# Performance work log

Measured on AMD Instinct MI355X. Metric: run time of the kernel, lower is better.

Reference implementation:

```python
import jax, jax.numpy as jnp
import numpy as np

D_MODEL = 1024
NUM_HEADS = 16
D_K = D_MODEL // NUM_HEADS


def setup_inputs() -> dict:
    key = jax.random.key(0)
    ks = jax.random.split(key, 11)
    s = 1.0 / np.sqrt(D_MODEL)
    inp = {
        "Q": jax.random.normal(ks[0], (2, 2048, D_MODEL), jnp.float32),
        "K": jax.random.normal(ks[1], (2, 2048, D_MODEL), jnp.float32),
        "V": jax.random.normal(ks[2], (2, 2048, D_MODEL), jnp.float32),
        "W_q": jax.random.uniform(ks[3], (D_MODEL, D_MODEL), jnp.float32, -s, s),
        "b_q": jax.random.uniform(ks[4], (D_MODEL,), jnp.float32, -s, s),
        "W_k": jax.random.uniform(ks[5], (D_MODEL, D_MODEL), jnp.float32, -s, s),
        "b_k": jax.random.uniform(ks[6], (D_MODEL,), jnp.float32, -s, s),
        "W_v": jax.random.uniform(ks[7], (D_MODEL, D_MODEL), jnp.float32, -s, s),
        "b_v": jax.random.uniform(ks[8], (D_MODEL,), jnp.float32, -s, s),
        "W_o": jax.random.uniform(ks[9], (D_MODEL, D_MODEL), jnp.float32, -s, s),
        "b_o": jax.random.uniform(ks[10], (D_MODEL,), jnp.float32, -s, s),
    }
    return inp


def reference(Q, K, V, W_q, b_q, W_k, b_k, W_v, b_v, W_o, b_o):
    B, S, _ = Q.shape
    # Linear projections (torch Linear: x @ W.T + b; W here stored as [in, out])
    q = Q @ W_q + b_q
    k = K @ W_k + b_k
    v = V @ W_v + b_v
    # split heads -> [B, H, S, d_k]
    q = q.reshape(B, S, NUM_HEADS, D_K).transpose(0, 2, 1, 3)
    k = k.reshape(B, S, NUM_HEADS, D_K).transpose(0, 2, 1, 3)
    v = v.reshape(B, S, NUM_HEADS, D_K).transpose(0, 2, 1, 3)
    scale = 1.0 / np.sqrt(D_K).astype(np.float32)
    scores = jnp.einsum('bhqd,bhkd->bhqk', q, k) * scale  # [B,H,S,S]
    probs = jax.nn.softmax(scores, axis=-1)
    attn = jnp.einsum('bhqk,bhkd->bhqd', probs, v)  # [B,H,S,d_k]
    attn = attn.transpose(0, 2, 1, 3).reshape(B, S, D_MODEL)
    return attn @ W_o + b_o
```

## Files before the change

kernel.cpp:

```cpp
#include <hip/hip_runtime.h>
#include <math.h>

#define SEQ   2048
#define DM    1024
#define NH    16
#define DK    64
#define MTOT  4096
#define QSCALE 0.18033688011112043f

typedef __bf16 bf16x8 __attribute__((ext_vector_type(8)));
typedef float  f32x4  __attribute__((ext_vector_type(4)));
typedef unsigned short u16;
typedef unsigned long long u64;

__device__ __forceinline__ u16 f2bf(float f) {
    unsigned int u = __float_as_uint(f);
    u += 0x7fff + ((u >> 16) & 1);
    return (u16)(u >> 16);
}

__device__ __forceinline__ void async16(const void* g, void* l) {
    __builtin_amdgcn_global_load_lds(
        (const __attribute__((address_space(1))) unsigned int*)(unsigned long long)g,
        (__attribute__((address_space(3))) unsigned int*)(unsigned int)(unsigned long long)l,
        16, 0, 0);
}

__device__ __forceinline__ bf16x8 ld16(const u16* p) {
    bf16x8 v;
    __builtin_memcpy(&v, p, 16);
    return v;
}
__device__ __forceinline__ bf16x8 ld8x2(const u16* p) {
    union { u64 q[2]; bf16x8 v; } u;
    __builtin_memcpy(&u.q[0], p, 8);
    __builtin_memcpy(&u.q[1], p + 4, 8);
    return u.v;
}
__device__ __forceinline__ void st8(u16* p, unsigned int lo, unsigned int hi) {
    u64 q = ((u64)hi << 32) | lo;
    __builtin_memcpy(p, &q, 8);
}

__global__ __launch_bounds__(256)
void cvt_in(const float* __restrict__ Q, const float* __restrict__ K,
            const float* __restrict__ V, u16* __restrict__ Qb,
            u16* __restrict__ Kb, u16* __restrict__ Vb)
{
    const float* src; u16* dst;
    if (blockIdx.z == 0)      { src = Q; dst = Qb; }
    else if (blockIdx.z == 1) { src = K; dst = Kb; }
    else                      { src = V; dst = Vb; }
    const size_t i = ((size_t)blockIdx.x * 256 + threadIdx.x) * 8;
    float4 a = *(const float4*)&src[i];
    float4 b = *(const float4*)&src[i + 4];
    uint4 o;
    o.x = (unsigned)f2bf(a.x) | ((unsigned)f2bf(a.y) << 16);
    o.y = (unsigned)f2bf(a.z) | ((unsigned)f2bf(a.w) << 16);
    o.z = (unsigned)f2bf(b.x) | ((unsigned)f2bf(b.y) << 16);
    o.w = (unsigned)f2bf(b.z) | ((unsigned)f2bf(b.w) << 16);
    *(uint4*)&dst[i] = o;
}

__global__ __launch_bounds__(256)
void cvt_wt(const float* __restrict__ Wq, const float* __restrict__ Wk,
            const float* __restrict__ Wv, const float* __restrict__ Wo,
            u16* __restrict__ Tq, u16* __restrict__ Tk,
            u16* __restrict__ Tv, u16* __restrict__ To)
{
    const float* W; u16* Wt;
    if (blockIdx.z == 0)      { W = Wq; Wt = Tq; }
    else if (blockIdx.z == 1) { W = Wk; Wt = Tk; }
    else if (blockIdx.z == 2) { W = Wv; Wt = Tv; }
    else                      { W = Wo; Wt = To; }
    __shared__ float Ts[64][65];
    const int t = threadIdx.x;
    const int k0 = blockIdx.x * 64, n0 = blockIdx.y * 64;
#pragma unroll
    for (int p = 0; p < 4; ++p) {
        const int flat = t + p * 256;
        const int r = flat >> 4, c4 = (flat & 15) * 4;
        float4 v = *(const float4*)&W[(size_t)(k0 + r) * DM + n0 + c4];
        Ts[r][c4 + 0] = v.x; Ts[r][c4 + 1] = v.y;
        Ts[r][c4 + 2] = v.z; Ts[r][c4 + 3] = v.w;
    }
    __syncthreads();
#pragma unroll
    for (int p = 0; p < 2; ++p) {
        const int flat = t + p * 256;
        const int n = flat >> 3, kc = (flat & 7) * 8;
        uint4 o;
        o.x = (unsigned)f2bf(Ts[kc + 0][n]) | ((unsigned)f2bf(Ts[kc + 1][n]) << 16);
        o.y = (unsigned)f2bf(Ts[kc + 2][n]) | ((unsigned)f2bf(Ts[kc + 3][n]) << 16);
        o.z = (unsigned)f2bf(Ts[kc + 4][n]) | ((unsigned)f2bf(Ts[kc + 5][n]) << 16);
        o.w = (unsigned)f2bf(Ts[kc + 6][n]) | ((unsigned)f2bf(Ts[kc + 7][n]) << 16);
        *(uint4*)&Wt[(size_t)(n0 + n) * DM + k0 + kc] = o;
    }
}

template <int SCATTER>
__device__ __forceinline__ void gemm_core(const u16* __restrict__ A,
                                          const u16* __restrict__ Wt,
                                          const float* __restrict__ bias,
                                          void* __restrict__ Out, float scale)
{
    __shared__ u16 As[2][128 * 32];
    __shared__ u16 Bs[2][128 * 32];

    const int tid = threadIdx.x;
    const int lane = tid & 63;
    const int wv = __builtin_amdgcn_readfirstlane(tid >> 6);
    const int wm = wv >> 1, wn = wv & 1;
    const int lane15 = lane & 15, quad = lane >> 4;
    const int row0 = blockIdx.x * 128, col0 = blockIdx.y * 128;

    const int arow = lane >> 2;
    const int acol = (lane & 3) * 8;

    f32x4 acc[4][4];
#pragma unroll
    for (int i = 0; i < 4; ++i)
#pragma unroll
        for (int j = 0; j < 4; ++j) acc[i][j] = (f32x4)0.f;

    for (int k0 = 0; k0 < DM; k0 += 64) {
#pragma unroll
        for (int p = 0; p < 2; ++p) {
#pragma unroll
            for (int cc = 0; cc < 2; ++cc) {
                const int c = 2 * wv + cc;
                async16(&A[(size_t)(row0 + c * 16 + arow) * DM + k0 + p * 32 + acol],
                        &As[p][c * 512]);
                async16(&Wt[(size_t)(col0 + c * 16 + arow) * DM + k0 + p * 32 + acol],
                        &Bs[p][c * 512]);
            }
        }
        __syncthreads();

#pragma unroll
        for (int kk = 0; kk < 2; ++kk) {
            bf16x8 af[4];
#pragma unroll
            for (int mi = 0; mi < 4; ++mi)
                af[mi] = ld16(&As[kk][(wm * 64 + mi * 16 + lane15) * 32 + quad * 8]);
#pragma unroll
            for (int ni = 0; ni < 4; ++ni) {
                bf16x8 bfrag = ld16(&Bs[kk][(wn * 64 + ni * 16 + lane15) * 32 + quad * 8]);
#pragma unroll
                for (int mi = 0; mi < 4; ++mi)
                    acc[mi][ni] = __builtin_amdgcn_mfma_f32_16x16x32_bf16(
                        af[mi], bfrag, acc[mi][ni], 0, 0, 0);
            }
        }
        __syncthreads();
    }

#pragma unroll
    for (int mi = 0; mi < 4; ++mi) {
        const int mbase = row0 + wm * 64 + mi * 16 + quad * 4;
#pragma unroll
        for (int ni = 0; ni < 4; ++ni) {
            const int n = col0 + wn * 64 + ni * 16 + lane15;
            const float bz = bias[n];
            if (SCATTER == 1) {
                const int h = n >> 6, dk = n & 63;
#pragma unroll
                for (int r = 0; r < 4; ++r) {
                    const int mm = mbase + r;
                    const int b_ = mm >> 11, s = mm & 2047;
                    ((u16*)Out)[(((size_t)(b_ * NH + h)) * SEQ + s) * DK + dk] =
                        f2bf((acc[mi][ni][r] + bz) * scale);
                }
            } else if (SCATTER == 2) {
                const int h = n >> 6, dk = n & 63;
                const int b_ = mbase >> 11, s0 = mbase & 2047;
                u64 q = (u64)f2bf((acc[mi][ni][0] + bz) * scale)
                      | ((u64)f2bf((acc[mi][ni][1] + bz) * scale) << 16)
                      | ((u64)f2bf((acc[mi][ni][2] + bz) * scale) << 32)
                      | ((u64)f2bf((acc[mi][ni][3] + bz) * scale) << 48);
                u16* dst = (u16*)Out +
                    (((size_t)(b_ * NH + h)) * DK + dk) * SEQ + s0;
                __builtin_memcpy(dst, &q, 8);
            } else {
#pragma unroll
                for (int r = 0; r < 4; ++r) {
                    const int mm = mbase + r;
                    ((float*)Out)[(size_t)mm * DM + n] = acc[mi][ni][r] + bz;
                }
            }
        }
    }
}

__global__ __launch_bounds__(256)
void qkv_gemm(const u16* __restrict__ Qb, const u16* __restrict__ Kb,
              const u16* __restrict__ Vb,
              const u16* __restrict__ Tq, const u16* __restrict__ Tk,
              const u16* __restrict__ Tv,
              const float* __restrict__ bq, const float* __restrict__ bk,
              const float* __restrict__ bv,
              u16* __restrict__ qw, u16* __restrict__ kw, u16* __restrict__ vtw)
{
    if (blockIdx.z == 0)      gemm_core<1>(Qb, Tq, bq, qw, QSCALE);
    else if (blockIdx.z == 1) gemm_core<1>(Kb, Tk, bk, kw, 1.0f);
    else                      gemm_core<2>(Vb, Tv, bv, vtw, 1.0f);
}

__global__ __launch_bounds__(256)
void out_gemm(const u16* __restrict__ A, const u16* __restrict__ Wt,
              const float* __restrict__ bias, float* __restrict__ Out)
{
    __shared__ u16 As[2][128 * 32];
    __shared__ u16 Bs[2][64 * 32];

    const int tid = threadIdx.x;
    const int lane = tid & 63;
    const int wv = __builtin_amdgcn_readfirstlane(tid >> 6);
    const int wm = wv >> 1, wn = wv & 1;
    const int lane15 = lane & 15, quad = lane >> 4;
    const int row0 = blockIdx.x * 128, col0 = blockIdx.y * 64;

    const int arow = lane >> 2;
    const int acol = (lane & 3) * 8;

    f32x4 acc[4][2];
#pragma unroll
    for (int i = 0; i < 4; ++i)
#pragma unroll
        for (int j = 0; j < 2; ++j) acc[i][j] = (f32x4)0.f;

    for (int k0 = 0; k0 < DM; k0 += 64) {
#pragma unroll
        for (int p = 0; p < 2; ++p) {
#pragma unroll
            for (int cc = 0; cc < 2; ++cc) {
                const int c = 2 * wv + cc;
                async16(&A[(size_t)(row0 + c * 16 + arow) * DM + k0 + p * 32 + acol],
                        &As[p][c * 512]);
            }
            async16(&Wt[(size_t)(col0 + wv * 16 + arow) * DM + k0 + p * 32 + acol],
                    &Bs[p][wv * 512]);
        }
        __syncthreads();

#pragma unroll
        for (int kk = 0; kk < 2; ++kk) {
            bf16x8 af[4];
#pragma unroll
            for (int mi = 0; mi < 4; ++mi)
                af[mi] = ld16(&As[kk][(wm * 64 + mi * 16 + lane15) * 32 + quad * 8]);
#pragma unroll
            for (int ni = 0; ni < 2; ++ni) {
                bf16x8 bfrag = ld16(&Bs[kk][(wn * 32 + ni * 16 + lane15) * 32 + quad * 8]);
#pragma unroll
                for (int mi = 0; mi < 4; ++mi)
                    acc[mi][ni] = __builtin_amdgcn_mfma_f32_16x16x32_bf16(
                        af[mi], bfrag, acc[mi][ni], 0, 0, 0);
            }
        }
        __syncthreads();
    }

#pragma unroll
    for (int mi = 0; mi < 4; ++mi) {
        const int mbase = row0 + wm * 64 + mi * 16 + quad * 4;
#pragma unroll
        for (int ni = 0; ni < 2; ++ni) {
            const int n = col0 + wn * 32 + ni * 16 + lane15;
            const float bz = bias[n];
#pragma unroll
            for (int r = 0; r < 4; ++r)
                Out[(size_t)(mbase + r) * DM + n] = acc[mi][ni][r] + bz;
        }
    }
}

__global__ __launch_bounds__(128, 3)
void attn_mfma(const u16* __restrict__ qw, const u16* __restrict__ kw,
               const u16* __restrict__ vt, u16* __restrict__ opart,
               float* __restrict__ lw)
{
    __shared__ u16 Ks[64 * 68];
    __shared__ u16 Vts[64 * 68];
    __shared__ u16 Ps[2][32 * 68];

    const int tid = threadIdx.x;
    const int lane = tid & 63;
    const int wv = tid >> 6;
    const int lane15 = lane & 15, quad = lane >> 4;

    const int flat = blockIdx.x;
    const int xcd = flat & 7;
    const int rest = flat >> 3;
    const int bh = xcd * 4 + (rest & 3);
    const int qt = (rest >> 2) & 31;
    const int ks = rest >> 7;
    const int q0 = qt * 64;
    const int c0beg = ks * 1024;
    const size_t base = (size_t)bh * SEQ * DK;

    bf16x8 qa[2][2];
#pragma unroll
    for (int mi = 0; mi < 2; ++mi)
#pragma unroll
        for (int kk = 0; kk < 2; ++kk)
            qa[mi][kk] = ld16(&qw[base +
                (size_t)(q0 + wv * 32 + mi * 16 + lane15) * DK + kk * 32 + quad * 8]);

    u16* Pw = &Ps[wv][0];

    f32x4 o_acc[2][4];
    float lpart[8];
#pragma unroll
    for (int mi = 0; mi < 2; ++mi)
#pragma unroll
        for (int nd = 0; nd < 4; ++nd) o_acc[mi][nd] = (f32x4)0.f;
#pragma unroll
    for (int r = 0; r < 8; ++r) lpart[r] = 0.f;

    const int sr = tid >> 1;
    const int sh = (tid & 1) * 32;

#pragma unroll
    for (int j = 0; j < 4; ++j) {
        const int c = sh + j * 8;
        const int cb = (c & 15) * 4 + (c >> 4);
        uint4 kv = *(const uint4*)&kw[base + (size_t)(c0beg + sr) * DK + c];
        st8(&Ks[sr * 68 + c], kv.x, kv.y);
        st8(&Ks[sr * 68 + c + 4], kv.z, kv.w);
        union { uint4 u; u16 s[8]; } vu;
        vu.u = *(const uint4*)&vt[base + (size_t)sr * SEQ + c0beg + c];
#pragma unroll
        for (int e = 0; e < 8; ++e) Vts[sr * 68 + cb + 4 * e] = vu.s[e];
    }
    __syncthreads();

    for (int it = 0; it < 16; ++it) {
        const int c0 = c0beg + it * 64;
        uint4 kpre[4], vpre[4];
        const bool more = (it < 15);
        if (more) {
#pragma unroll
            for (int j = 0; j < 4; ++j) {
                const int c = sh + j * 8;
                kpre[j] = *(const uint4*)&kw[base + (size_t)(c0 + 64 + sr) * DK + c];
                vpre[j] = *(const uint4*)&vt[base + (size_t)sr * SEQ + c0 + 64 + c];
            }
        }

        f32x4 s_acc[2][4];
#pragma unroll
        for (int mi = 0; mi < 2; ++mi)
#pragma unroll
            for (int ni = 0; ni < 4; ++ni) s_acc[mi][ni] = (f32x4)0.f;
#pragma unroll
        for (int ni = 0; ni < 4; ++ni)
#pragma unroll
            for (int kk = 0; kk < 2; ++kk) {
                bf16x8 kb = ld8x2(&Ks[(ni * 16 + lane15) * 68 + kk * 32 + quad * 8]);
#pragma unroll
                for (int mi = 0; mi < 2; ++mi)
                    s_acc[mi][ni] = __builtin_amdgcn_mfma_f32_16x16x32_bf16(
                        qa[mi][kk], kb, s_acc[mi][ni], 0, 0, 0);
            }

#pragma unroll
        for (int mi = 0; mi < 2; ++mi)
#pragma unroll
            for (int r = 0; r < 4; ++r) {
                unsigned int u[4];
#pragma unroll
                for (int ni = 0; ni < 4; ++ni) {
                    const float p = __builtin_amdgcn_exp2f(s_acc[mi][ni][r]);
                    lpart[mi * 4 + r] += p;
                    u[ni] = __float_as_uint(p) + 0x8000u;
                }
                const unsigned int lo = __builtin_amdgcn_perm(u[1], u[0], 0x07060302u);
                const unsigned int hi = __builtin_amdgcn_perm(u[3], u[2], 0x07060302u);
                st8(&Pw[(mi * 16 + quad * 4 + r) * 68 + lane15 * 4], lo, hi);
            }

        bf16x8 pa[2][2];
#pragma unroll
        for (int mi = 0; mi < 2; ++mi)
#pragma unroll
            for (int kk = 0; kk < 2; ++kk)
                pa[mi][kk] = ld8x2(&Pw[(mi * 16 + lane15) * 68 + kk * 32 + quad * 8]);
#pragma unroll
        for (int nd = 0; nd < 4; ++nd)
#pragma unroll
            for (int kk = 0; kk < 2; ++kk) {
                bf16x8 vb = ld8x2(&Vts[(nd * 16 + lane15) * 68 + kk * 32 + quad * 8]);
#pragma unroll
                for (int mi = 0; mi < 2; ++mi)
                    o_acc[mi][nd] = __builtin_amdgcn_mfma_f32_16x16x32_bf16(
                        pa[mi][kk], vb, o_acc[mi][nd], 0, 0, 0);
            }
        __syncthreads();

        if (more) {
#pragma unroll
            for (int j = 0; j < 4; ++j) {
                const int c = sh + j * 8;
                const int cb = (c & 15) * 4 + (c >> 4);
                st8(&Ks[sr * 68 + c], kpre[j].x, kpre[j].y);
                st8(&Ks[sr * 68 + c + 4], kpre[j].z, kpre[j].w);
                union { uint4 u; u16 s[8]; } vu;
                vu.u = vpre[j];
#pragma unroll
                for (int e = 0; e < 8; ++e) Vts[sr * 68 + cb + 4 * e] = vu.s[e];
            }
        }
        __syncthreads();
    }

    const size_t obase = ((size_t)(ks * 32 + bh)) * SEQ;
#pragma unroll
    for (int mi = 0; mi < 2; ++mi)
#pragma unroll
        for (int r = 0; r < 4; ++r) {
            const int s = q0 + wv * 32 + mi * 16 + quad * 4 + r;
            float l = lpart[mi * 4 + r];
            l += __shfl_xor(l, 1);
            l += __shfl_xor(l, 2);
            l += __shfl_xor(l, 4);
            l += __shfl_xor(l, 8);
            if (lane15 == 0)
                lw[(size_t)(ks * 32 + bh) * SEQ + s] = l;
#pragma unroll
            for (int nd = 0; nd < 4; ++nd)
                opart[(obase + s) * DK + nd * 16 + lane15] = f2bf(o_acc[mi][nd][r]);
        }
}

__global__ __launch_bounds__(256)
void attn_combine(const u16* __restrict__ opart, const float* __restrict__ lw,
                  u16* __restrict__ attnb)
{
    const int flat = blockIdx.x * 256 + threadIdx.x;
    const int dv = (flat & 7) * 8;
    const int s  = (flat >> 3) & 2047;
    const int bh = flat >> 14;
    const size_t i0 = ((size_t)bh * SEQ + s) * DK + dv;
    const size_t i1 = i0 + (size_t)32 * SEQ * DK;
    uint4 a = *(const uint4*)&opart[i0];
    uint4 b = *(const uint4*)&opart[i1];
    const float l = lw[(size_t)bh * SEQ + s] + lw[(size_t)(32 + bh) * SEQ + s];
    const float inv = 1.f / l;
    unsigned int au[4] = {a.x, a.y, a.z, a.w};
    unsigned int bu[4] = {b.x, b.y, b.z, b.w};
    unsigned int ou[4];
#pragma unroll
    for (int j = 0; j < 4; ++j) {
        const float e0 = __uint_as_float(au[j] << 16) + __uint_as_float(bu[j] << 16);
        const float e1 = __uint_as_float(au[j] & 0xffff0000u) +
                         __uint_as_float(bu[j] & 0xffff0000u);
        ou[j] = (unsigned)f2bf(e0 * inv) | ((unsigned)f2bf(e1 * inv) << 16);
    }
    const int b_ = bh >> 4, h = bh & 15;
    uint4 o; o.x = ou[0]; o.y = ou[1]; o.z = ou[2]; o.w = ou[3];
    *(uint4*)&attnb[((size_t)b_ * SEQ + s) * DM + h * DK + dv] = o;
}

extern "C" void kernel_launch(void* const* d_in, const int* in_sizes, int n_in,
                              void* d_out, int out_size, void* d_ws, size_t ws_size,
                              hipStream_t stream)
{
    const float* Q  = (const float*)d_in[0];
    const float* K  = (const float*)d_in[1];
    const float* V  = (const float*)d_in[2];
    const float* Wq = (const float*)d_in[3];
    const float* bq = (const float*)d_in[4];
    const float* Wk = (const float*)d_in[5];
    const float* bk = (const float*)d_in[6];
    const float* Wv = (const float*)d_in[7];
    const float* bv = (const float*)d_in[8];
    const float* Wo = (const float*)d_in[9];
    const float* bo = (const float*)d_in[10];
    float* out = (float*)d_out;

    const size_t MB = 1024 * 1024;
    char* w8 = (char*)d_ws;
    u16* Qbf = (u16*)(w8 + 0 * MB);
    u16* Kbf = (u16*)(w8 + 8 * MB);
    u16* Vbf = (u16*)(w8 + 16 * MB);
    u16* Wtq = (u16*)(w8 + 24 * MB);
    u16* Wtk = (u16*)(w8 + 26 * MB);
    u16* Wtv = (u16*)(w8 + 28 * MB);
    u16* Wto = (u16*)(w8 + 30 * MB);
    u16* qw  = (u16*)(w8 + 32 * MB);
    u16* kw  = (u16*)(w8 + 40 * MB);
    u16* vtw = (u16*)(w8 + 48 * MB);
    u16* opart = Kbf;
    float* lwb = (float*)(w8 + 56 * MB);
    u16* attnb = Qbf;

    cvt_in<<<dim3(2048, 1, 3), 256, 0, stream>>>(Q, K, V, Qbf, Kbf, Vbf);
    cvt_wt<<<dim3(16, 16, 4), 256, 0, stream>>>(Wq, Wk, Wv, Wo,
                                                Wtq, Wtk, Wtv, Wto);
    qkv_gemm<<<dim3(32, 8, 3), 256, 0, stream>>>(Qbf, Kbf, Vbf, Wtq, Wtk, Wtv,
                                                 bq, bk, bv, qw, kw, vtw);
    attn_mfma<<<2048, 128, 0, stream>>>(qw, kw, vtw, opart, lwb);
    attn_combine<<<2048, 256, 0, stream>>>(opart, lwb, attnb);
    out_gemm<<<dim3(32, 16), 256, 0, stream>>>(attnb, Wto, bo, out);
}
```

Before: 249.9 us.

## Transpose QK^T to keep P in registers, double-buffer K/V, shrink GEMM k-step

The attention kernel now computes S^T by swapping MFMA operands (K as A, Q as B). The exp'd probabilities then land directly in the register layout the PV MFMA needs, which removes the per-wave LDS round trip for P. K/V tiles are double-buffered with a padded stride of 72 and a permuted V slot layout, allowing 16-byte LDS reads and one barrier per iteration instead of two. Occupancy is lowered to 2 blocks. Separately, both projection GEMMs drop from a 64-wide k-step with two LDS stages to a 32-wide k-step with one stage, which halves shared memory but doubles the number of barriers.

```diff
diff --git a/kernel.cpp b/kernel.cpp
--- a/kernel.cpp
+++ b/kernel.cpp
@@ -30,12 +30,6 @@
     bf16x8 v;
     __builtin_memcpy(&v, p, 16);
     return v;
-}
-__device__ __forceinline__ bf16x8 ld8x2(const u16* p) {
-    union { u64 q[2]; bf16x8 v; } u;
-    __builtin_memcpy(&u.q[0], p, 8);
-    __builtin_memcpy(&u.q[1], p + 4, 8);
-    return u.v;
 }
 __device__ __forceinline__ void st8(u16* p, unsigned int lo, unsigned int hi) {
     u64 q = ((u64)hi << 32) | lo;
@@ -104,8 +98,8 @@
                                           const float* __restrict__ bias,
                                           void* __restrict__ Out, float scale)
 {
-    __shared__ u16 As[2][128 * 32];
-    __shared__ u16 Bs[2][128 * 32];
+    __shared__ u16 As[128 * 32];
+    __shared__ u16 Bs[128 * 32];
 
     const int tid = threadIdx.x;
     const int lane = tid & 63;
@@ -123,34 +117,28 @@
 #pragma unroll
         for (int j = 0; j < 4; ++j) acc[i][j] = (f32x4)0.f;
 
-    for (int k0 = 0; k0 < DM; k0 += 64) {
-#pragma unroll
-        for (int p = 0; p < 2; ++p) {
-#pragma unroll
-            for (int cc = 0; cc < 2; ++cc) {
-                const int c = 2 * wv + cc;
-                async16(&A[(size_t)(row0 + c * 16 + arow) * DM + k0 + p * 32 + acol],
-                        &As[p][c * 512]);
-                async16(&Wt[(size_t)(col0 + c * 16 + arow) * DM + k0 + p * 32 + acol],
-                        &Bs[p][c * 512]);
-            }
+    for (int k0 = 0; k0 < DM; k0 += 32) {
+#pragma unroll
+        for (int cc = 0; cc < 2; ++cc) {
+            const int c = 2 * wv + cc;
+            async16(&A[(size_t)(row0 + c * 16 + arow) * DM + k0 + acol],
+                    &As[c * 512]);
+            async16(&Wt[(size_t)(col0 + c * 16 + arow) * DM + k0 + acol],
+                    &Bs[c * 512]);
         }
         __syncthreads();
 
-#pragma unroll
-        for (int kk = 0; kk < 2; ++kk) {
-            bf16x8 af[4];
+        bf16x8 af[4];
+#pragma unroll
+        for (int mi = 0; mi < 4; ++mi)
+            af[mi] = ld16(&As[(wm * 64 + mi * 16 + lane15) * 32 + quad * 8]);
+#pragma unroll
+        for (int ni = 0; ni < 4; ++ni) {
+            bf16x8 bfrag = ld16(&Bs[(wn * 64 + ni * 16 + lane15) * 32 + quad * 8]);
 #pragma unroll
             for (int mi = 0; mi < 4; ++mi)
-                af[mi] = ld16(&As[kk][(wm * 64 + mi * 16 + lane15) * 32 + quad * 8]);
-#pragma unroll
-            for (int ni = 0; ni < 4; ++ni) {
-                bf16x8 bfrag = ld16(&Bs[kk][(wn * 64 + ni * 16 + lane15) * 32 + quad * 8]);
-#pragma unroll
-                for (int mi = 0; mi < 4; ++mi)
-                    acc[mi][ni] = __builtin_amdgcn_mfma_f32_16x16x32_bf16(
-                        af[mi], bfrag, acc[mi][ni], 0, 0, 0);
-            }
+                acc[mi][ni] = __builtin_amdgcn_mfma_f32_16x16x32_bf16(
+                    af[mi], bfrag, acc[mi][ni], 0, 0, 0);
         }
         __syncthreads();
     }
@@ -210,8 +198,8 @@
 void out_gemm(const u16* __restrict__ A, const u16* __restrict__ Wt,
               const float* __restrict__ bias, float* __restrict__ Out)
 {
-    __shared__ u16 As[2][128 * 32];
-    __shared__ u16 Bs[2][64 * 32];
+    __shared__ u16 As[128 * 32];
+    __shared__ u16 Bs[64 * 32];
 
     const int tid = threadIdx.x;
     const int lane = tid & 63;
@@ -229,34 +217,28 @@
 #pragma unroll
         for (int j = 0; j < 2; ++j) acc[i][j] = (f32x4)0.f;
 
-    for (int k0 = 0; k0 < DM; k0 += 64) {
-#pragma unroll
-        for (int p = 0; p < 2; ++p) {
-#pragma unroll
-            for (int cc = 0; cc < 2; ++cc) {
-                const int c = 2 * wv + cc;
-                async16(&A[(size_t)(row0 + c * 16 + arow) * DM + k0 + p * 32 + acol],
-                        &As[p][c * 512]);
-            }
-            async16(&Wt[(size_t)(col0 + wv * 16 + arow) * DM + k0 + p * 32 + acol],
-                    &Bs[p][wv * 512]);
-        }
+    for (int k0 = 0; k0 < DM; k0 += 32) {
+#pragma unroll
+        for (int cc = 0; cc < 2; ++cc) {
+            const int c = 2 * wv + cc;
+            async16(&A[(size_t)(row0 + c * 16 + arow) * DM + k0 + acol],
+                    &As[c * 512]);
+        }
+        async16(&Wt[(size_t)(col0 + wv * 16 + arow) * DM + k0 + acol],
+                &Bs[wv * 512]);
         __syncthreads();
 
-#pragma unroll
-        for (int kk = 0; kk < 2; ++kk) {
-            bf16x8 af[4];
+        bf16x8 af[4];
+#pragma unroll
+        for (int mi = 0; mi < 4; ++mi)
+            af[mi] = ld16(&As[(wm * 64 + mi * 16 + lane15) * 32 + quad * 8]);
+#pragma unroll
+        for (int ni = 0; ni < 2; ++ni) {
+            bf16x8 bfrag = ld16(&Bs[(wn * 32 + ni * 16 + lane15) * 32 + quad * 8]);
 #pragma unroll
             for (int mi = 0; mi < 4; ++mi)
-                af[mi] = ld16(&As[kk][(wm * 64 + mi * 16 + lane15) * 32 + quad * 8]);
-#pragma unroll
-            for (int ni = 0; ni < 2; ++ni) {
-                bf16x8 bfrag = ld16(&Bs[kk][(wn * 32 + ni * 16 + lane15) * 32 + quad * 8]);
-#pragma unroll
-                for (int mi = 0; mi < 4; ++mi)
-                    acc[mi][ni] = __builtin_amdgcn_mfma_f32_16x16x32_bf16(
-                        af[mi], bfrag, acc[mi][ni], 0, 0, 0);
-            }
+                acc[mi][ni] = __builtin_amdgcn_mfma_f32_16x16x32_bf16(
+                    af[mi], bfrag, acc[mi][ni], 0, 0, 0);
         }
         __syncthreads();
     }
@@ -275,14 +257,13 @@
     }
 }
 
-__global__ __launch_bounds__(128, 3)
+__global__ __launch_bounds__(128, 2)
 void attn_mfma(const u16* __restrict__ qw, const u16* __restrict__ kw,
                const u16* __restrict__ vt, u16* __restrict__ opart,
                float* __restrict__ lw)
 {
-    __shared__ u16 Ks[64 * 68];
-    __shared__ u16 Vts[64 * 68];
-    __shared__ u16 Ps[2][32 * 68];
+    __shared__ u16 Ks[2][64 * 72];
+    __shared__ u16 Vts[2][64 * 72];
 
     const int tid = threadIdx.x;
     const int lane = tid & 63;
@@ -299,137 +280,146 @@
     const int c0beg = ks * 1024;
     const size_t base = (size_t)bh * SEQ * DK;
 
-    bf16x8 qa[2][2];
+    bf16x8 qb[2][2];
 #pragma unroll
     for (int mi = 0; mi < 2; ++mi)
 #pragma unroll
         for (int kk = 0; kk < 2; ++kk)
-            qa[mi][kk] = ld16(&qw[base +
+            qb[mi][kk] = ld16(&qw[base +
                 (size_t)(q0 + wv * 32 + mi * 16 + lane15) * DK + kk * 32 + quad * 8]);
 
-    u16* Pw = &Ps[wv][0];
-
     f32x4 o_acc[2][4];
-    float lpart[8];
-#pragma unroll
-    for (int mi = 0; mi < 2; ++mi)
+    float lpart[2];
+#pragma unroll
+    for (int mi = 0; mi < 2; ++mi) {
+        lpart[mi] = 0.f;
 #pragma unroll
         for (int nd = 0; nd < 4; ++nd) o_acc[mi][nd] = (f32x4)0.f;
-#pragma unroll
-    for (int r = 0; r < 8; ++r) lpart[r] = 0.f;
+    }
 
     const int sr = tid >> 1;
     const int sh = (tid & 1) * 32;
 
+    int vslot[4];
 #pragma unroll
     for (int j = 0; j < 4; ++j) {
-        const int c = sh + j * 8;
-        const int cb = (c & 15) * 4 + (c >> 4);
-        uint4 kv = *(const uint4*)&kw[base + (size_t)(c0beg + sr) * DK + c];
-        st8(&Ks[sr * 68 + c], kv.x, kv.y);
-        st8(&Ks[sr * 68 + c + 4], kv.z, kv.w);
-        union { uint4 u; u16 s[8]; } vu;
-        vu.u = *(const uint4*)&vt[base + (size_t)sr * SEQ + c0beg + c];
-#pragma unroll
-        for (int e = 0; e < 8; ++e) Vts[sr * 68 + cb + 4 * e] = vu.s[e];
+        const int c8 = sh + j * 8;
+        const int a = c8 >> 4, b = (c8 >> 2) & 3;
+        vslot[j] = (a >> 1) * 32 + b * 8 + (a & 1) * 4;
+    }
+
+#pragma unroll
+    for (int j = 0; j < 4; ++j) {
+        const int c8 = sh + j * 8;
+        uint4 kv = *(const uint4*)&kw[base + (size_t)(c0beg + sr) * DK + c8];
+        st8(&Ks[0][sr * 72 + c8], kv.x, kv.y);
+        st8(&Ks[0][sr * 72 + c8 + 4], kv.z, kv.w);
+        uint4 vv = *(const uint4*)&vt[base + (size_t)sr * SEQ + c0beg + c8];
+        st8(&Vts[0][sr * 72 + vslot[j]], vv.x, vv.y);
+        st8(&Vts[0][sr * 72 + vslot[j] + 8], vv.z, vv.w);
     }
     __syncthreads();
 
     for (int it = 0; it < 16; ++it) {
-        const int c0 = c0beg + it * 64;
+        const int cur = it & 1;
+        const u16* Kc = &Ks[cur][0];
+        const u16* Vc = &Vts[cur][0];
+
         uint4 kpre[4], vpre[4];
         const bool more = (it < 15);
         if (more) {
+            const int cn = c0beg + (it + 1) * 64;
 #pragma unroll
             for (int j = 0; j < 4; ++j) {
-                const int c = sh + j * 8;
-                kpre[j] = *(const uint4*)&kw[base + (size_t)(c0 + 64 + sr) * DK + c];
-                vpre[j] = *(const uint4*)&vt[base + (size_t)sr * SEQ + c0 + 64 + c];
-            }
-        }
-
-        f32x4 s_acc[2][4];
+                const int c8 = sh + j * 8;
+                kpre[j] = *(const uint4*)&kw[base + (size_t)(cn + sr) * DK + c8];
+                vpre[j] = *(const uint4*)&vt[base + (size_t)sr * SEQ + cn + c8];
+            }
+        }
+
+        f32x4 sT[2][4];
 #pragma unroll
         for (int mi = 0; mi < 2; ++mi)
 #pragma unroll
-            for (int ni = 0; ni < 4; ++ni) s_acc[mi][ni] = (f32x4)0.f;
-#pragma unroll
-        for (int ni = 0; ni < 4; ++ni)
+            for (int ki = 0; ki < 4; ++ki) sT[mi][ki] = (f32x4)0.f;
+#pragma unroll
+        for (int ki = 0; ki < 4; ++ki)
 #pragma unroll
             for (int kk = 0; kk < 2; ++kk) {
-                bf16x8 kb = ld8x2(&Ks[(ni * 16 + lane15) * 68 + kk * 32 + quad * 8]);
+                bf16x8 ka = ld16(&Kc[(ki * 16 + lane15) * 72 + kk * 32 + quad * 8]);
 #pragma unroll
                 for (int mi = 0; mi < 2; ++mi)
-                    s_acc[mi][ni] = __builtin_amdgcn_mfma_f32_16x16x32_bf16(
-                        qa[mi][kk], kb, s_acc[mi][ni], 0, 0, 0);
-            }
-
-#pragma unroll
-        for (int mi = 0; mi < 2; ++mi)
-#pragma unroll
-            for (int r = 0; r < 4; ++r) {
+                    sT[mi][ki] = __builtin_amdgcn_mfma_f32_16x16x32_bf16(
+                        ka, qb[mi][kk], sT[mi][ki], 0, 0, 0);
+            }
+
+        bf16x8 pa[2][2];
+#pragma unroll
+        for (int mi = 0; mi < 2; ++mi) {
+            unsigned int ulo[4], uhi[4];
+#pragma unroll
+            for (int ki = 0; ki < 4; ++ki) {
                 unsigned int u[4];
 #pragma unroll
-                for (int ni = 0; ni < 4; ++ni) {
-                    const float p = __builtin_amdgcn_exp2f(s_acc[mi][ni][r]);
-                    lpart[mi * 4 + r] += p;
-                    u[ni] = __float_as_uint(p) + 0x8000u;
+                for (int r = 0; r < 4; ++r) {
+                    const float p = __builtin_amdgcn_exp2f(sT[mi][ki][r]);
+                    lpart[mi] += p;
+                    u[r] = __float_as_uint(p) + 0x8000u;
                 }
-                const unsigned int lo = __builtin_amdgcn_perm(u[1], u[0], 0x07060302u);
-                const unsigned int hi = __builtin_amdgcn_perm(u[3], u[2], 0x07060302u);
-                st8(&Pw[(mi * 16 + quad * 4 + r) * 68 + lane15 * 4], lo, hi);
-            }
-
-        bf16x8 pa[2][2];
-#pragma unroll
-        for (int mi = 0; mi < 2; ++mi)
-#pragma unroll
-            for (int kk = 0; kk < 2; ++kk)
-                pa[mi][kk] = ld8x2(&Pw[(mi * 16 + lane15) * 68 + kk * 32 + quad * 8]);
+                ulo[ki] = __builtin_amdgcn_perm(u[1], u[0], 0x07060302u);
+                uhi[ki] = __builtin_amdgcn_perm(u[3], u[2], 0x07060302u);
+            }
+#pragma unroll
+            for (int kk = 0; kk < 2; ++kk) {
+                union { uint4 u; bf16x8 v; } pk;
+                pk.u.x = ulo[2 * kk];     pk.u.y = uhi[2 * kk];
+                pk.u.z = ulo[2 * kk + 1]; pk.u.w = uhi[2 * kk + 1];
+                pa[mi][kk] = pk.v;
+            }
+        }
+
 #pragma unroll
         for (int nd = 0; nd < 4; ++nd)
 #pragma unroll
             for (int kk = 0; kk < 2; ++kk) {
-                bf16x8 vb = ld8x2(&Vts[(nd * 16 + lane15) * 68 + kk * 32 + quad * 8]);
+                bf16x8 vb = ld16(&Vc[(nd * 16 + lane15) * 72 + kk * 32 + quad * 8]);
 #pragma unroll
                 for (int mi = 0; mi < 2; ++mi)
                     o_acc[mi][nd] = __builtin_amdgcn_mfma_f32_16x16x32_bf16(
                         pa[mi][kk], vb, o_acc[mi][nd], 0, 0, 0);
             }
+
+        if (more) {
+            const int nxt = cur ^ 1;
+#pragma unroll
+            for (int j = 0; j < 4; ++j) {
+                const int c8 = sh + j * 8;
+                st8(&Ks[nxt][sr * 72 + c8], kpre[j].x, kpre[j].y);
+                st8(&Ks[nxt][sr * 72 + c8 + 4], kpre[j].z, kpre[j].w);
+                st8(&Vts[nxt][sr * 72 + vslot[j]], vpre[j].x, vpre[j].y);
+                st8(&Vts[nxt][sr * 72 + vslot[j] + 8], vpre[j].z, vpre[j].w);
+            }
+        }
         __syncthreads();
-
-        if (more) {
-#pragma unroll
-            for (int j = 0; j < 4; ++j) {
-                const int c = sh + j * 8;
-                const int cb = (c & 15) * 4 + (c >> 4);
-                st8(&Ks[sr * 68 + c], kpre[j].x, kpre[j].y);
-                st8(&Ks[sr * 68 + c + 4], kpre[j].z, kpre[j].w);
-                union { uint4 u; u16 s[8]; } vu;
-                vu.u = vpre[j];
-#pragma unroll
-                for (int e = 0; e < 8; ++e) Vts[sr * 68 + cb + 4 * e] = vu.s[e];
-            }
-        }
-        __syncthreads();
-    }
-
-    const size_t obase = ((size_t)(ks * 32 + bh)) * SEQ;
+    }
+
+    const size_t rowbase = (size_t)(ks * 32 + bh) * SEQ;
+#pragma unroll
+    for (int mi = 0; mi < 2; ++mi) {
+        float l = lpart[mi];
+        l += __shfl_xor(l, 16);
+        l += __shfl_xor(l, 32);
+        if (quad == 0)
+            lw[rowbase + q0 + wv * 32 + mi * 16 + lane15] = l;
+    }
 #pragma unroll
     for (int mi = 0; mi < 2; ++mi)
 #pragma unroll
         for (int r = 0; r < 4; ++r) {
             const int s = q0 + wv * 32 + mi * 16 + quad * 4 + r;
-            float l = lpart[mi * 4 + r];
-            l += __shfl_xor(l, 1);
-            l += __shfl_xor(l, 2);
-            l += __shfl_xor(l, 4);
-            l += __shfl_xor(l, 8);
-            if (lane15 == 0)
-                lw[(size_t)(ks * 32 + bh) * SEQ + s] = l;
 #pragma unroll
             for (int nd = 0; nd < 4; ++nd)
-                opart[(obase + s) * DK + nd * 16 + lane15] = f2bf(o_acc[mi][nd][r]);
+                opart[(rowbase + s) * DK + nd * 16 + lane15] = f2bf(o_acc[mi][nd][r]);
         }
 }
 
```

After: 226.6 us. 9.3% less time.
